# Optimization experiments

Measured on AMD Instinct MI355X. Metric: run time of the kernel, lower is better.

The kernel has to match this reference:

```python
import jax, jax.numpy as jnp
import numpy as np

N, E, D, H, C, ED = 30000, 300000, 256, 8, 32, 32
HID = H * C  # 256 = hidden_channels


def setup_inputs() -> dict:
    key = jax.random.key(0)
    ks = jax.random.split(key, 14)
    w = lambda k, shp, fan: (jax.random.normal(k, shp, jnp.float32) / np.sqrt(fan)).astype(jnp.float32)
    return {
        "x": jax.random.normal(ks[0], (N, D), jnp.float32),
        "edge_index": jax.random.randint(ks[1], (2, E), 0, N, jnp.int32),
        "edge_attr": jax.random.normal(ks[2], (E, ED), jnp.float32),
        # TransformerConv params (PyG: q/k/v Linears have bias; lin_edge & lin_skip bias=False)
        "Wq": w(ks[3], (D, HID), D), "bq": 0.01 * jax.random.normal(ks[4], (HID,), jnp.float32),
        "Wk": w(ks[5], (D, HID), D), "bk": 0.01 * jax.random.normal(ks[6], (HID,), jnp.float32),
        "Wv": w(ks[7], (D, HID), D), "bv": 0.01 * jax.random.normal(ks[8], (HID,), jnp.float32),
        "We": w(ks[9], (ED, HID), ED),
        "Wskip": w(ks[10], (D, HID), D),
        # MLP([HID, HID, HID], gelu-tanh, plain_last=False): two Linear+act layers
        "W1": w(ks[11], (HID, HID), HID), "b1": jnp.zeros((HID,), jnp.float32),
        "W2": w(ks[12], (HID, HID), HID), "b2": jnp.zeros((HID,), jnp.float32),
    }


def reference(x, edge_index, edge_attr, Wq, bq, Wk, bk, Wv, bv, We, Wskip, W1, b1, W2, b2):
    src, dst = edge_index[0], edge_index[1]  # message flows src -> dst
    q = (x @ Wq + bq).reshape(N, H, C)
    k = (x @ Wk + bk).reshape(N, H, C)
    v = (x @ Wv + bv).reshape(N, H, C)
    e = (edge_attr @ We).reshape(E, H, C)
    k_e = k[src] + e                               # [E,H,C]
    v_e = v[src] + e                               # [E,H,C]
    logits = jnp.einsum('ehc,ehc->eh', q[dst], k_e) / np.sqrt(C)  # [E,H]
    # segment softmax over incoming edges of each dst node
    m = jax.ops.segment_max(logits, dst, num_segments=N)          # [N,H]
    a = jnp.exp(logits - m[dst])
    denom = jax.ops.segment_sum(a, dst, num_segments=N)           # [N,H]
    alpha = a / (denom[dst] + 1e-16)                              # [E,H]
    agg = jax.ops.segment_sum(alpha[:, :, None] * v_e, dst, num_segments=N)  # [N,H,C]
    out = agg.reshape(N, HID) + x @ Wskip          # concat heads + root skip
    # residual MLP: x + gelu(gelu(x W1 + b1) W2 + b2)
    h = jax.nn.gelu(out @ W1 + b1, approximate=True)
    h = jax.nn.gelu(h @ W2 + b2, approximate=True)
    return out + h
```

## Files before the change

### kernel.cpp

```cpp
#include <hip/hip_runtime.h>

#define NN 30000
#define NE 300000
#define HIDDEN 256

typedef __attribute__((ext_vector_type(8))) __bf16 bf16x8;
typedef __attribute__((ext_vector_type(4))) __bf16 bf16x4;
typedef __attribute__((ext_vector_type(4))) float float4v;

__device__ inline __bf16 f2bf(float f) {
  unsigned u = __builtin_bit_cast(unsigned, f);
  u += 0x7fffu + ((u >> 16) & 1u);
  unsigned short s = (unsigned short)(u >> 16);
  return __builtin_bit_cast(__bf16, s);
}
__device__ inline float bf2f(__bf16 b) {
  unsigned short s = __builtin_bit_cast(unsigned short, b);
  unsigned u = ((unsigned)s) << 16;
  return __builtin_bit_cast(float, u);
}
__device__ inline float gelu_tanh(float x) {
  float x3 = x * x * x;
  return 0.5f * x * (1.0f + tanhf(0.79788456080286536f * (x + 0.044715f * x3)));
}

__global__ __launch_bounds__(256) void prep_kernel(
    const float* __restrict__ Wq, const float* __restrict__ Wk, const float* __restrict__ Wv,
    const float* __restrict__ Wsk, const float* __restrict__ W1, const float* __restrict__ W2,
    const float* __restrict__ We, const float* __restrict__ bq, const float* __restrict__ bk,
    const float* __restrict__ bv, const float* __restrict__ x,
    __bf16* __restrict__ WTall, __bf16* __restrict__ WT1, __bf16* __restrict__ WT2,
    float* __restrict__ ball, float* __restrict__ WeT, __bf16* __restrict__ xb) {
  const int b = blockIdx.x;
  const int tid = threadIdx.x;
  if (b < 1792) {
    const int region = b >> 8;
    const int idx = ((b & 255) << 8) | tid;
    const int k = idx & 255, n = idx >> 8;
    float v;
    if (region == 3) {
      const int h = n >> 5, d = n & 31;
      const float* wq = Wq + (size_t)k * 256 + h * 32;
      const float* we = We + (size_t)d * 256 + h * 32;
      float s = 0.f;
#pragma unroll
      for (int c = 0; c < 32; ++c) s += wq[c] * we[c];
      v = s;
    } else {
      const float* W = (region == 0) ? Wq : (region == 1) ? Wk : (region == 2) ? Wv
                     : (region == 4) ? Wsk : (region == 5) ? W1 : W2;
      v = W[(size_t)k * 256 + n];
    }
    const __bf16 bv16 = f2bf(v);
    if (region < 5) WTall[(size_t)region * 65536 + idx] = bv16;
    else if (region == 5) WT1[idx] = bv16;
    else WT2[idx] = bv16;
  } else if (b < 1797) {
    const int j = (b - 1792) * 256 + tid;
    if (j < 1280) {
      float v = 0.f;
      if (j < 256) v = bq[j];
      else if (j < 512) v = bk[j - 256];
      else if (j < 768) v = bv[j - 512];
      else if (j < 1024) {
        const int col = j - 768, h = col >> 5, d = col & 31;
        const float* bqh = bq + h * 32;
        const float* we = We + (size_t)d * 256 + h * 32;
        float s = 0.f;
#pragma unroll
        for (int c = 0; c < 32; ++c) s += bqh[c] * we[c];
        v = s;
      }
      ball[j] = v;
    }
  } else if (b < 1829) {
    const int idx = (b - 1797) * 256 + tid;
    const int ch = idx >> 5, d = idx & 31;
    WeT[idx] = We[(size_t)d * 256 + ch];
  } else {
    const int t = (b - 1829) * 256 + tid;
    if (t < NN * 256 / 8) {
      const float* p = x + (size_t)t * 8;
      float4v f0 = *(const float4v*)(p);
      float4v f1 = *(const float4v*)(p + 4);
      bf16x8 o;
#pragma unroll
      for (int j = 0; j < 4; ++j) { o[j] = f2bf(f0[j]); o[j + 4] = f2bf(f1[j]); }
      *(bf16x8*)(xb + (size_t)t * 8) = o;
    }
  }
}

__global__ void zero_int_kernel(int* __restrict__ p, int n) {
  int i = blockIdx.x * 256 + threadIdx.x;
  if (i < n) p[i] = 0;
}

__global__ void count_deg_kernel(const int* __restrict__ dst, int* __restrict__ deg, int E) {
  int e = blockIdx.x * 256 + threadIdx.x;
  if (e < E) atomicAdd(&deg[dst[e]], 1);
}

__global__ __launch_bounds__(1024) void scan_kernel(const int* __restrict__ deg,
                                                    int* __restrict__ offs, int n) {
  __shared__ int part[1024];
  const int tid = threadIdx.x;
  const int per = (n + 1023) / 1024;
  const int base = tid * per;
  int s = 0;
  for (int j = 0; j < per; ++j) {
    int i = base + j;
    if (i < n) s += deg[i];
  }
  part[tid] = s;
  __syncthreads();
  for (int st = 1; st < 1024; st <<= 1) {
    int t = (tid >= st) ? part[tid - st] : 0;
    __syncthreads();
    part[tid] += t;
    __syncthreads();
  }
  int run = (tid > 0) ? part[tid - 1] : 0;
  for (int j = 0; j < per; ++j) {
    int i = base + j;
    if (i < n) { offs[i] = run; run += deg[i]; }
  }
  if (tid == 1023) offs[n] = part[1023];
}

__global__ void scatter_kernel(const int* __restrict__ srcIn, const int* __restrict__ dstIn,
                               const int* __restrict__ offs, int* __restrict__ cursor,
                               int* __restrict__ srcs, int* __restrict__ eids, int E) {
  int e = blockIdx.x * 256 + threadIdx.x;
  if (e >= E) return;
  int d = dstIn[e];
  int p = atomicAdd(&cursor[d], 1);
  int o = offs[d] + p;
  srcs[o] = srcIn[e];
  eids[o] = e;
}

__global__ void gather_ea_kernel(const float* __restrict__ ea, const int* __restrict__ eids,
                                 __bf16* __restrict__ eaC, int E) {
  int t = blockIdx.x * 256 + threadIdx.x;
  if (t >= E * 4) return;
  int o = t >> 2, part = t & 3;
  int e = eids[o];
  const float* src = ea + (size_t)e * 32 + part * 8;
  float4v f0 = *(const float4v*)(src);
  float4v f1 = *(const float4v*)(src + 4);
  bf16x8 b;
#pragma unroll
  for (int j = 0; j < 4; ++j) { b[j] = f2bf(f0[j]); b[j + 4] = f2bf(f1[j]); }
  *(bf16x8*)(eaC + (size_t)o * 32 + part * 8) = b;
}

template <int GX, int EPI, int MODE>
__global__ __launch_bounds__(256) void gemm_k4(
    const __bf16* __restrict__ A, const __bf16* __restrict__ Wt,
    const float* __restrict__ bias,
    float* __restrict__ Yf, __bf16* __restrict__ Ybf,
    __bf16* __restrict__ QGp, __bf16* __restrict__ KVp,
    const float* __restrict__ resid, int M, int gyTiles) {
  __shared__ char smem[128 * 264 * 2];
  __bf16* Bs = (__bf16*)smem;
  const int bid = blockIdx.x;
  const int stripe = bid / (8 * GX);
  const int rem = bid % (8 * GX);
  const int y8 = rem % 8;
  const int xt = rem / 8;
  const int y = stripe * 8 + y8;
  if (y >= gyTiles) return;
  const int n0 = xt * 128;

  {
    const int t = threadIdx.x;
#pragma unroll
    for (int i = 0; i < 16; ++i) {
      int g = i * 256 + t;
      int row = g >> 5;
      int c16 = g & 31;
      bf16x8 v = *(const bf16x8*)(Wt + (size_t)(n0 + row) * 256 + c16 * 8);
      *(bf16x8*)(Bs + row * 264 + c16 * 8) = v;
    }
  }
  __syncthreads();

  const int lane = threadIdx.x & 63;
  const int w = threadIdx.x >> 6;
  const int r = lane & 15;
  const int q = lane >> 4;
  const int mw = y * 128 + w * 32;
  int ar0 = mw + r;      if (ar0 >= M) ar0 = M - 1;
  int ar1 = mw + 16 + r; if (ar1 >= M) ar1 = M - 1;
  const int kq = q * 8;

  float4v acc[2][8];
#pragma unroll
  for (int i = 0; i < 2; ++i)
#pragma unroll
    for (int t = 0; t < 8; ++t) acc[i][t] = (float4v){0.f, 0.f, 0.f, 0.f};

#pragma unroll
  for (int kk = 0; kk < 256; kk += 32) {
    const int ka = kk + kq;
    bf16x8 a0 = *(const bf16x8*)(A + (size_t)ar0 * 256 + ka);
    bf16x8 a1 = *(const bf16x8*)(A + (size_t)ar1 * 256 + ka);
    bf16x8 b[8];
#pragma unroll
    for (int t = 0; t < 8; ++t)
      b[t] = *(const bf16x8*)(Bs + (t * 16 + r) * 264 + ka);
#pragma unroll
    for (int t = 0; t < 8; ++t) {
      acc[0][t] = __builtin_amdgcn_mfma_f32_16x16x32_bf16(a0, b[t], acc[0][t], 0, 0, 0);
      acc[1][t] = __builtin_amdgcn_mfma_f32_16x16x32_bf16(a1, b[t], acc[1][t], 0, 0, 0);
    }
  }
  __syncthreads();

  float* cs = (float*)smem + w * 4224;
#pragma unroll
  for (int t = 0; t < 8; ++t) {
    const int col = n0 + t * 16 + r;
    const float bb = bias ? bias[col] : 0.0f;
#pragma unroll
    for (int i2 = 0; i2 < 2; ++i2)
#pragma unroll
      for (int ii = 0; ii < 4; ++ii) {
        float v = acc[i2][t][ii] + bb;
        if constexpr (EPI == 2 || EPI == 3) v = gelu_tanh(v);
        cs[(i2 * 16 + q * 4 + ii) * 132 + t * 16 + r] = v;
      }
  }

  constexpr int NSTR = GX * 128;
  const int p = n0 >> 8;
  const int cbase = n0 & 255;
  __bf16* dstI = (p == 0 || p == 3) ? QGp : KVp;
  const int moff = (p >= 2) ? 4 : 0;
#pragma unroll
  for (int i = 0; i < 16; ++i) {
    const int rl = i * 2 + (lane >> 5);
    const int row = mw + rl;
    const int c4 = (lane & 31) * 4;
    float4v v = *(const float4v*)(cs + rl * 132 + c4);
    if (row < M) {
      if constexpr (MODE == 1) {
        if (p == 4) {
          *(float4v*)(Yf + (size_t)row * 256 + cbase + c4) = v;
        } else {
          bf16x4 b4;
          b4[0] = f2bf(v[0]); b4[1] = f2bf(v[1]); b4[2] = f2bf(v[2]); b4[3] = f2bf(v[3]);
          const int c = cbase + c4;
          *(bf16x4*)(dstI + (size_t)row * 512 + 2 * c + moff) = b4;
        }
      } else if constexpr (EPI == 1) {
        *(float4v*)(Yf + (size_t)row * NSTR + n0 + c4) = v;
      } else if constexpr (EPI == 3) {
        float4v rr = *(const float4v*)(resid + (size_t)row * NSTR + n0 + c4);
        v[0] += rr[0]; v[1] += rr[1]; v[2] += rr[2]; v[3] += rr[3];
        *(float4v*)(Yf + (size_t)row * NSTR + n0 + c4) = v;
      } else {
        bf16x4 b4;
        b4[0] = f2bf(v[0]); b4[1] = f2bf(v[1]); b4[2] = f2bf(v[2]); b4[3] = f2bf(v[3]);
        *(bf16x4*)(Ybf + (size_t)row * NSTR + n0 + c4) = b4;
      }
    }
  }
}

__global__ __launch_bounds__(256) void attn_kernel(
    const __bf16* __restrict__ QG, const __bf16* __restrict__ KV,
    const __bf16* __restrict__ eaC,
    const int* __restrict__ offs, const int* __restrict__ srcs,
    float* __restrict__ OUT, __bf16* __restrict__ AE) {
  __shared__ float sdn[4][64];
  __shared__ float sav[4][64][4], sae[4][64][4];
  const int lane = threadIdx.x & 63;
  const int w = threadIdx.x >> 6;
  const int n = blockIdx.x;
  const int c0 = lane * 4;
  const int sub = lane & 7;

  const bf16x8 qg = *(const bf16x8*)(QG + (size_t)n * 512 + lane * 8);
  const float q0 = bf2f(qg[0]), q1 = bf2f(qg[1]), q2 = bf2f(qg[2]), q3 = bf2f(qg[3]);
  const float g0 = bf2f(qg[4]), g1 = bf2f(qg[5]), g2 = bf2f(qg[6]), g3 = bf2f(qg[7]);

  float denom = 0.f;
  float4v accv = {0.f, 0.f, 0.f, 0.f};
  float4v acce = {0.f, 0.f, 0.f, 0.f};
  const int beg = offs[n], end = offs[n + 1];
  for (int i = beg + w; i < end; i += 4) {
    const int sn = srcs[i];
    const bf16x8 kv = *(const bf16x8*)(KV + (size_t)sn * 512 + lane * 8);
    const bf16x4 e4 = *(const bf16x4*)(eaC + (size_t)i * 32 + sub * 4);
    const float e0 = bf2f(e4[0]), e1 = bf2f(e4[1]), e2 = bf2f(e4[2]), e3 = bf2f(e4[3]);
    float part = q0 * bf2f(kv[0]) + q1 * bf2f(kv[1]) + q2 * bf2f(kv[2]) + q3 * bf2f(kv[3])
               + g0 * e0 + g1 * e1 + g2 * e2 + g3 * e3;
    part += __shfl_xor(part, 1);
    part += __shfl_xor(part, 2);
    part += __shfl_xor(part, 4);
    const float wgt = __expf(part * 0.17677669529663687f);
    denom += wgt;
    accv[0] += wgt * bf2f(kv[4]);
    accv[1] += wgt * bf2f(kv[5]);
    accv[2] += wgt * bf2f(kv[6]);
    accv[3] += wgt * bf2f(kv[7]);
    acce[0] += wgt * e0;
    acce[1] += wgt * e1;
    acce[2] += wgt * e2;
    acce[3] += wgt * e3;
  }
  sdn[w][lane] = denom;
#pragma unroll
  for (int j = 0; j < 4; ++j) { sav[w][lane][j] = accv[j]; sae[w][lane][j] = acce[j]; }
  __syncthreads();
  if (w == 0) {
    float D = 0.f;
    float4v av = {0.f, 0.f, 0.f, 0.f};
    float4v ae = {0.f, 0.f, 0.f, 0.f};
#pragma unroll
    for (int ww = 0; ww < 4; ++ww) {
      D += sdn[ww][lane];
#pragma unroll
      for (int j = 0; j < 4; ++j) { av[j] += sav[ww][lane][j]; ae[j] += sae[ww][lane][j]; }
    }
    const float inv = 1.0f / (D + 1e-16f);
    float4v o = *(const float4v*)(OUT + (size_t)n * 256 + c0);
#pragma unroll
    for (int j = 0; j < 4; ++j) o[j] += av[j] * inv;
    *(float4v*)(OUT + (size_t)n * 256 + c0) = o;
    bf16x4 aeb;
    aeb[0] = f2bf(ae[0] * inv); aeb[1] = f2bf(ae[1] * inv);
    aeb[2] = f2bf(ae[2] * inv); aeb[3] = f2bf(ae[3] * inv);
    *(bf16x4*)(AE + (size_t)n * 256 + c0) = aeb;
  }
}

__global__ __launch_bounds__(256) void post_kernel(
    const __bf16* __restrict__ AE, const float* __restrict__ WeT,
    float* __restrict__ OUT, __bf16* __restrict__ OUTh) {
  const int lane = threadIdx.x & 63;
  const int wave = threadIdx.x >> 6;
  const int c0 = lane * 4;
  const int hg = lane >> 3;

  float4v w4[4][8];
#pragma unroll
  for (int j = 0; j < 4; ++j)
#pragma unroll
    for (int s = 0; s < 8; ++s)
      w4[j][s] = *(const float4v*)(WeT + (size_t)(c0 + j) * 32 + s * 4);

  const int nbase = blockIdx.x * 64;
  for (int it = 0; it < 16; ++it) {
    const int n = nbase + it * 4 + wave;
    if (n >= NN) return;
    const __bf16* aerow = AE + (size_t)n * HIDDEN + hg * 32;
    float aef[32];
#pragma unroll
    for (int t = 0; t < 4; ++t) {
      bf16x8 a8 = *(const bf16x8*)(aerow + t * 8);
#pragma unroll
      for (int j = 0; j < 8; ++j) aef[t * 8 + j] = bf2f(a8[j]);
    }
    float4v o = *(const float4v*)(OUT + (size_t)n * HIDDEN + c0);
#pragma unroll
    for (int j = 0; j < 4; ++j) {
      float s = 0.f;
#pragma unroll
      for (int g = 0; g < 8; ++g) {
        s += aef[g * 4 + 0] * w4[j][g][0] + aef[g * 4 + 1] * w4[j][g][1]
           + aef[g * 4 + 2] * w4[j][g][2] + aef[g * 4 + 3] * w4[j][g][3];
      }
      o[j] += s;
    }
    *(float4v*)(OUT + (size_t)n * HIDDEN + c0) = o;
    bf16x4 ob;
    ob[0] = f2bf(o[0]); ob[1] = f2bf(o[1]); ob[2] = f2bf(o[2]); ob[3] = f2bf(o[3]);
    *(bf16x4*)(OUTh + (size_t)n * HIDDEN + c0) = ob;
  }
}

extern "C" void kernel_launch(void* const* d_in, const int* in_sizes, int n_in,
                              void* d_out, int out_size, void* d_ws, size_t ws_size,
                              hipStream_t stream) {
  (void)in_sizes; (void)n_in; (void)out_size; (void)ws_size;
  const float* x   = (const float*)d_in[0];
  const int*   ei  = (const int*)d_in[1];
  const float* ea  = (const float*)d_in[2];
  const float* Wq  = (const float*)d_in[3];
  const float* bq  = (const float*)d_in[4];
  const float* Wk  = (const float*)d_in[5];
  const float* bk  = (const float*)d_in[6];
  const float* Wv  = (const float*)d_in[7];
  const float* bv  = (const float*)d_in[8];
  const float* We  = (const float*)d_in[9];
  const float* Wsk = (const float*)d_in[10];
  const float* W1  = (const float*)d_in[11];
  const float* b1  = (const float*)d_in[12];
  const float* W2  = (const float*)d_in[13];
  const float* b2  = (const float*)d_in[14];
  float* out = (float*)d_out;

  char* ws = (char*)d_ws;
  size_t off = 0;
  auto alloc = [&](size_t bytes) -> char* {
    off = (off + 255) & ~(size_t)255;
    char* p = ws + off;
    off += bytes;
    return p;
  };
  __bf16* QG   = (__bf16*)alloc((size_t)NN * 512 * 2);
  __bf16* KV   = (__bf16*)alloc((size_t)NN * 512 * 2);
  __bf16* xb   = (__bf16*)alloc((size_t)NN * 256 * 2);
  __bf16* AE   = (__bf16*)alloc((size_t)NN * 256 * 2);
  __bf16* OUTh = (__bf16*)alloc((size_t)NN * 256 * 2);
  __bf16* eaC  = (__bf16*)alloc((size_t)NE * 32 * 2);
  __bf16* WTall = (__bf16*)alloc((size_t)1280 * 256 * 2);
  __bf16* WT1  = (__bf16*)alloc(256 * 256 * 2);
  __bf16* WT2  = (__bf16*)alloc(256 * 256 * 2);
  float*  ball = (float*)alloc(1280 * 4);
  float*  WeT  = (float*)alloc(256 * 32 * 4);
  int* deg    = (int*)alloc((size_t)2 * NN * 4);
  int* cursor = deg + NN;
  int* offs   = (int*)alloc((size_t)(NN + 1) * 4);
  int* srcs   = (int*)alloc((size_t)NE * 4);
  int* eids   = (int*)alloc((size_t)NE * 4);
  __bf16* H1 = AE;

  const int* srcIn = ei;
  const int* dstIn = ei + NE;

  const int prepBlocks = 1829 + (NN * 256 / 8 + 255) / 256;
  prep_kernel<<<prepBlocks, 256, 0, stream>>>(Wq, Wk, Wv, Wsk, W1, W2, We, bq, bk, bv, x,
                                              WTall, WT1, WT2, ball, WeT, xb);

  zero_int_kernel<<<(2 * NN + 255) / 256, 256, 0, stream>>>(deg, 2 * NN);
  count_deg_kernel<<<(NE + 255) / 256, 256, 0, stream>>>(dstIn, deg, NE);
  scan_kernel<<<1, 1024, 0, stream>>>(deg, offs, NN);
  scatter_kernel<<<(NE + 255) / 256, 256, 0, stream>>>(srcIn, dstIn, offs, cursor, srcs, eids, NE);
  gather_ea_kernel<<<(NE * 4 + 255) / 256, 256, 0, stream>>>(ea, eids, eaC, NE);

  const int gy = (NN + 127) / 128;
  const int stripes = (gy + 7) / 8;
  gemm_k4<10, 0, 1><<<stripes * 80, 256, 0, stream>>>(
      xb, WTall, ball, out, nullptr, QG, KV, nullptr, NN, gy);

  attn_kernel<<<NN, 256, 0, stream>>>(QG, KV, eaC, offs, srcs, out, AE);

  post_kernel<<<(NN + 63) / 64, 256, 0, stream>>>(AE, WeT, out, OUTh);

  gemm_k4<2, 2, 0><<<stripes * 16, 256, 0, stream>>>(
      OUTh, WT1, b1, nullptr, H1, nullptr, nullptr, nullptr, NN, gy);
  gemm_k4<2, 3, 0><<<stripes * 16, 256, 0, stream>>>(
      H1, WT2, b2, out, nullptr, nullptr, nullptr, out, NN, gy);
}
```

Measured before the change: 404.4 us.

## Parallelize CSR scan, pack src/eid pairs, drop edge gather, one wave per node attention

Replaces the single-block serial scan with a three-kernel multi-block prefix sum, and folds degree zeroing into the prep kernel. The scatter step now writes packed (src, eid) pairs, and the separate bf16 edge-attribute gather kernel is removed. The attention kernel reads fp32 edge_attr directly by edge id. It now assigns one wave per destination node instead of four waves per node, which removes the shared-memory reduction and block barrier, and unrolls the edge loop by two using exp2. In exchange, edge-attribute reads become random and twice as wide, and high-degree nodes are processed serially by a single wave.

```diff
diff --git a/kernel.cpp b/kernel.cpp
--- a/kernel.cpp
+++ b/kernel.cpp
@@ -24,13 +24,15 @@
   return 0.5f * x * (1.0f + tanhf(0.79788456080286536f * (x + 0.044715f * x3)));
 }
 
+#define PREP_XB_END (1829 + (NN * 32 + 255) / 256)
 __global__ __launch_bounds__(256) void prep_kernel(
     const float* __restrict__ Wq, const float* __restrict__ Wk, const float* __restrict__ Wv,
     const float* __restrict__ Wsk, const float* __restrict__ W1, const float* __restrict__ W2,
     const float* __restrict__ We, const float* __restrict__ bq, const float* __restrict__ bk,
     const float* __restrict__ bv, const float* __restrict__ x,
     __bf16* __restrict__ WTall, __bf16* __restrict__ WT1, __bf16* __restrict__ WT2,
-    float* __restrict__ ball, float* __restrict__ WeT, __bf16* __restrict__ xb) {
+    float* __restrict__ ball, float* __restrict__ WeT, __bf16* __restrict__ xb,
+    int* __restrict__ degz) {
   const int b = blockIdx.x;
   const int tid = threadIdx.x;
   if (b < 1792) {
@@ -77,7 +79,7 @@
     const int idx = (b - 1797) * 256 + tid;
     const int ch = idx >> 5, d = idx & 31;
     WeT[idx] = We[(size_t)d * 256 + ch];
-  } else {
+  } else if (b < PREP_XB_END) {
     const int t = (b - 1829) * 256 + tid;
     if (t < NN * 256 / 8) {
       const float* p = x + (size_t)t * 8;
@@ -88,12 +90,10 @@
       for (int j = 0; j < 4; ++j) { o[j] = f2bf(f0[j]); o[j + 4] = f2bf(f1[j]); }
       *(bf16x8*)(xb + (size_t)t * 8) = o;
     }
-  }
-}
-
-__global__ void zero_int_kernel(int* __restrict__ p, int n) {
-  int i = blockIdx.x * 256 + threadIdx.x;
-  if (i < n) p[i] = 0;
+  } else {
+    const int idx = (b - PREP_XB_END) * 256 + tid;
+    if (idx < 2 * NN) degz[idx] = 0;
+  }
 }
 
 __global__ void count_deg_kernel(const int* __restrict__ dst, int* __restrict__ deg, int E) {
@@ -101,58 +101,61 @@
   if (e < E) atomicAdd(&deg[dst[e]], 1);
 }
 
-__global__ __launch_bounds__(1024) void scan_kernel(const int* __restrict__ deg,
-                                                    int* __restrict__ offs, int n) {
-  __shared__ int part[1024];
-  const int tid = threadIdx.x;
-  const int per = (n + 1023) / 1024;
-  const int base = tid * per;
-  int s = 0;
-  for (int j = 0; j < per; ++j) {
-    int i = base + j;
-    if (i < n) s += deg[i];
-  }
-  part[tid] = s;
+__global__ __launch_bounds__(256) void deg_psum_kernel(const int* __restrict__ deg,
+                                                       int* __restrict__ psum, int n) {
+  int i = blockIdx.x * 256 + threadIdx.x;
+  int v = (i < n) ? deg[i] : 0;
+#pragma unroll
+  for (int s = 1; s < 64; s <<= 1) v += __shfl_xor(v, s);
+  __shared__ int ws[4];
+  if ((threadIdx.x & 63) == 0) ws[threadIdx.x >> 6] = v;
   __syncthreads();
-  for (int st = 1; st < 1024; st <<= 1) {
-    int t = (tid >= st) ? part[tid - st] : 0;
+  if (threadIdx.x == 0) psum[blockIdx.x] = ws[0] + ws[1] + ws[2] + ws[3];
+}
+
+__global__ __launch_bounds__(128) void psum_scan_kernel(int* __restrict__ psum,
+                                                        int* __restrict__ offs, int nb) {
+  __shared__ int tmp[128];
+  const int t = threadIdx.x;
+  int v = (t < nb) ? psum[t] : 0;
+  tmp[t] = v;
+  __syncthreads();
+  for (int s = 1; s < 128; s <<= 1) {
+    int u = (t >= s) ? tmp[t - s] : 0;
     __syncthreads();
-    part[tid] += t;
+    tmp[t] += u;
     __syncthreads();
   }
-  int run = (tid > 0) ? part[tid - 1] : 0;
-  for (int j = 0; j < per; ++j) {
-    int i = base + j;
-    if (i < n) { offs[i] = run; run += deg[i]; }
-  }
-  if (tid == 1023) offs[n] = part[1023];
+  if (t < nb) psum[t] = tmp[t] - v;
+  if (t == 0) offs[NN] = NE;
+}
+
+__global__ __launch_bounds__(256) void offs_kernel(const int* __restrict__ deg,
+                                                   const int* __restrict__ psum,
+                                                   int* __restrict__ offs, int n) {
+  __shared__ int tmp[256];
+  const int t = threadIdx.x;
+  const int i = blockIdx.x * 256 + t;
+  int v = (i < n) ? deg[i] : 0;
+  tmp[t] = v;
+  __syncthreads();
+  for (int s = 1; s < 256; s <<= 1) {
+    int u = (t >= s) ? tmp[t - s] : 0;
+    __syncthreads();
+    tmp[t] += u;
+    __syncthreads();
+  }
+  if (i < n) offs[i] = psum[blockIdx.x] + tmp[t] - v;
 }
 
 __global__ void scatter_kernel(const int* __restrict__ srcIn, const int* __restrict__ dstIn,
                                const int* __restrict__ offs, int* __restrict__ cursor,
-                               int* __restrict__ srcs, int* __restrict__ eids, int E) {
+                               int2* __restrict__ sed, int E) {
   int e = blockIdx.x * 256 + threadIdx.x;
   if (e >= E) return;
   int d = dstIn[e];
   int p = atomicAdd(&cursor[d], 1);
-  int o = offs[d] + p;
-  srcs[o] = srcIn[e];
-  eids[o] = e;
-}
-
-__global__ void gather_ea_kernel(const float* __restrict__ ea, const int* __restrict__ eids,
-                                 __bf16* __restrict__ eaC, int E) {
-  int t = blockIdx.x * 256 + threadIdx.x;
-  if (t >= E * 4) return;
-  int o = t >> 2, part = t & 3;
-  int e = eids[o];
-  const float* src = ea + (size_t)e * 32 + part * 8;
-  float4v f0 = *(const float4v*)(src);
-  float4v f1 = *(const float4v*)(src + 4);
-  bf16x8 b;
-#pragma unroll
-  for (int j = 0; j < 4; ++j) { b[j] = f2bf(f0[j]); b[j + 4] = f2bf(f1[j]); }
-  *(bf16x8*)(eaC + (size_t)o * 32 + part * 8) = b;
+  sed[offs[d] + p] = make_int2(srcIn[e], e);
 }
 
 template <int GX, int EPI, int MODE>
@@ -271,15 +274,13 @@
 
 __global__ __launch_bounds__(256) void attn_kernel(
     const __bf16* __restrict__ QG, const __bf16* __restrict__ KV,
-    const __bf16* __restrict__ eaC,
-    const int* __restrict__ offs, const int* __restrict__ srcs,
+    const float* __restrict__ ea, const int2* __restrict__ sed,
+    const int* __restrict__ offs,
     float* __restrict__ OUT, __bf16* __restrict__ AE) {
-  __shared__ float sdn[4][64];
-  __shared__ float sav[4][64][4], sae[4][64][4];
   const int lane = threadIdx.x & 63;
   const int w = threadIdx.x >> 6;
-  const int n = blockIdx.x;
-  const int c0 = lane * 4;
+  const int n = blockIdx.x * 4 + w;
+  if (n >= NN) return;
   const int sub = lane & 7;
 
   const bf16x8 qg = *(const bf16x8*)(QG + (size_t)n * 512 + lane * 8);
@@ -290,51 +291,66 @@
   float4v accv = {0.f, 0.f, 0.f, 0.f};
   float4v acce = {0.f, 0.f, 0.f, 0.f};
   const int beg = offs[n], end = offs[n + 1];
-  for (int i = beg + w; i < end; i += 4) {
-    const int sn = srcs[i];
-    const bf16x8 kv = *(const bf16x8*)(KV + (size_t)sn * 512 + lane * 8);
-    const bf16x4 e4 = *(const bf16x4*)(eaC + (size_t)i * 32 + sub * 4);
-    const float e0 = bf2f(e4[0]), e1 = bf2f(e4[1]), e2 = bf2f(e4[2]), e3 = bf2f(e4[3]);
-    float part = q0 * bf2f(kv[0]) + q1 * bf2f(kv[1]) + q2 * bf2f(kv[2]) + q3 * bf2f(kv[3])
-               + g0 * e0 + g1 * e1 + g2 * e2 + g3 * e3;
-    part += __shfl_xor(part, 1);
-    part += __shfl_xor(part, 2);
-    part += __shfl_xor(part, 4);
-    const float wgt = __expf(part * 0.17677669529663687f);
-    denom += wgt;
-    accv[0] += wgt * bf2f(kv[4]);
-    accv[1] += wgt * bf2f(kv[5]);
-    accv[2] += wgt * bf2f(kv[6]);
-    accv[3] += wgt * bf2f(kv[7]);
-    acce[0] += wgt * e0;
-    acce[1] += wgt * e1;
-    acce[2] += wgt * e2;
-    acce[3] += wgt * e3;
-  }
-  sdn[w][lane] = denom;
-#pragma unroll
-  for (int j = 0; j < 4; ++j) { sav[w][lane][j] = accv[j]; sae[w][lane][j] = acce[j]; }
-  __syncthreads();
-  if (w == 0) {
-    float D = 0.f;
-    float4v av = {0.f, 0.f, 0.f, 0.f};
-    float4v ae = {0.f, 0.f, 0.f, 0.f};
-#pragma unroll
-    for (int ww = 0; ww < 4; ++ww) {
-      D += sdn[ww][lane];
-#pragma unroll
-      for (int j = 0; j < 4; ++j) { av[j] += sav[ww][lane][j]; ae[j] += sae[ww][lane][j]; }
-    }
-    const float inv = 1.0f / (D + 1e-16f);
-    float4v o = *(const float4v*)(OUT + (size_t)n * 256 + c0);
-#pragma unroll
-    for (int j = 0; j < 4; ++j) o[j] += av[j] * inv;
-    *(float4v*)(OUT + (size_t)n * 256 + c0) = o;
-    bf16x4 aeb;
-    aeb[0] = f2bf(ae[0] * inv); aeb[1] = f2bf(ae[1] * inv);
-    aeb[2] = f2bf(ae[2] * inv); aeb[3] = f2bf(ae[3] * inv);
-    *(bf16x4*)(AE + (size_t)n * 256 + c0) = aeb;
-  }
+  const float LSC = 0.25506589858f;
+
+  int i = beg;
+  for (; i + 2 <= end; i += 2) {
+    const int2 s0 = sed[i];
+    const int2 s1 = sed[i + 1];
+    const bf16x8 kv0 = *(const bf16x8*)(KV + (size_t)s0.x * 512 + lane * 8);
+    const float4v e0 = *(const float4v*)(ea + (size_t)s0.y * 32 + sub * 4);
+    const bf16x8 kv1 = *(const bf16x8*)(KV + (size_t)s1.x * 512 + lane * 8);
+    const float4v e1 = *(const float4v*)(ea + (size_t)s1.y * 32 + sub * 4);
+    float p0 = q0 * bf2f(kv0[0]) + q1 * bf2f(kv0[1]) + q2 * bf2f(kv0[2]) + q3 * bf2f(kv0[3])
+             + g0 * e0[0] + g1 * e0[1] + g2 * e0[2] + g3 * e0[3];
+    float p1 = q0 * bf2f(kv1[0]) + q1 * bf2f(kv1[1]) + q2 * bf2f(kv1[2]) + q3 * bf2f(kv1[3])
+             + g0 * e1[0] + g1 * e1[1] + g2 * e1[2] + g3 * e1[3];
+    p0 += __shfl_xor(p0, 1); p1 += __shfl_xor(p1, 1);
+    p0 += __shfl_xor(p0, 2); p1 += __shfl_xor(p1, 2);
+    p0 += __shfl_xor(p0, 4); p1 += __shfl_xor(p1, 4);
+    const float w0 = exp2f(p0 * LSC);
+    const float w1 = exp2f(p1 * LSC);
+    denom += w0 + w1;
+    accv[0] += w0 * bf2f(kv0[4]) + w1 * bf2f(kv1[4]);
+    accv[1] += w0 * bf2f(kv0[5]) + w1 * bf2f(kv1[5]);
+    accv[2] += w0 * bf2f(kv0[6]) + w1 * bf2f(kv1[6]);
+    accv[3] += w0 * bf2f(kv0[7]) + w1 * bf2f(kv1[7]);
+    acce[0] += w0 * e0[0] + w1 * e1[0];
+    acce[1] += w0 * e0[1] + w1 * e1[1];
+    acce[2] += w0 * e0[2] + w1 * e1[2];
+    acce[3] += w0 * e0[3] + w1 * e1[3];
+  }
+  if (i < end) {
+    const int2 s0 = sed[i];
+    const bf16x8 kv0 = *(const bf16x8*)(KV + (size_t)s0.x * 512 + lane * 8);
+    const float4v e0 = *(const float4v*)(ea + (size_t)s0.y * 32 + sub * 4);
+    float p0 = q0 * bf2f(kv0[0]) + q1 * bf2f(kv0[1]) + q2 * bf2f(kv0[2]) + q3 * bf2f(kv0[3])
+             + g0 * e0[0] + g1 * e0[1] + g2 * e0[2] + g3 * e0[3];
+    p0 += __shfl_xor(p0, 1);
+    p0 += __shfl_xor(p0, 2);
+    p0 += __shfl_xor(p0, 4);
+    const float w0 = exp2f(p0 * LSC);
+    denom += w0;
+    accv[0] += w0 * bf2f(kv0[4]);
+    accv[1] += w0 * bf2f(kv0[5]);
+    accv[2] += w0 * bf2f(kv0[6]);
+    accv[3] += w0 * bf2f(kv0[7]);
+    acce[0] += w0 * e0[0];
+    acce[1] += w0 * e0[1];
+    acce[2] += w0 * e0[2];
+    acce[3] += w0 * e0[3];
+  }
+
+  const float inv = 1.0f / (denom + 1e-16f);
+  const int c0 = lane * 4;
+  float4v o = *(const float4v*)(OUT + (size_t)n * 256 + c0);
+#pragma unroll
+  for (int j = 0; j < 4; ++j) o[j] += accv[j] * inv;
+  *(float4v*)(OUT + (size_t)n * 256 + c0) = o;
+  bf16x4 aeb;
+  aeb[0] = f2bf(acce[0] * inv); aeb[1] = f2bf(acce[1] * inv);
+  aeb[2] = f2bf(acce[2] * inv); aeb[3] = f2bf(acce[3] * inv);
+  *(bf16x4*)(AE + (size_t)n * 256 + c0) = aeb;
 }
 
 __global__ __launch_bounds__(256) void post_kernel(
@@ -416,7 +432,6 @@
   __bf16* xb   = (__bf16*)alloc((size_t)NN * 256 * 2);
   __bf16* AE   = (__bf16*)alloc((size_t)NN * 256 * 2);
   __bf16* OUTh = (__bf16*)alloc((size_t)NN * 256 * 2);
-  __bf16* eaC  = (__bf16*)alloc((size_t)NE * 32 * 2);
   __bf16* WTall = (__bf16*)alloc((size_t)1280 * 256 * 2);
   __bf16* WT1  = (__bf16*)alloc(256 * 256 * 2);
   __bf16* WT2  = (__bf16*)alloc(256 * 256 * 2);
@@ -425,29 +440,30 @@
   int* deg    = (int*)alloc((size_t)2 * NN * 4);
   int* cursor = deg + NN;
   int* offs   = (int*)alloc((size_t)(NN + 1) * 4);
-  int* srcs   = (int*)alloc((size_t)NE * 4);
-  int* eids   = (int*)alloc((size_t)NE * 4);
+  int* psum   = (int*)alloc(512);
+  int2* sed   = (int2*)alloc((size_t)NE * 8);
   __bf16* H1 = AE;
 
   const int* srcIn = ei;
   const int* dstIn = ei + NE;
 
-  const int prepBlocks = 1829 + (NN * 256 / 8 + 255) / 256;
+  const int prepBlocks = PREP_XB_END + (2 * NN + 255) / 256;
   prep_kernel<<<prepBlocks, 256, 0, stream>>>(Wq, Wk, Wv, Wsk, W1, W2, We, bq, bk, bv, x,
-                                              WTall, WT1, WT2, ball, WeT, xb);
-
-  zero_int_kernel<<<(2 * NN + 255) / 256, 256, 0, stream>>>(deg, 2 * NN);
+                                              WTall, WT1, WT2, ball, WeT, xb, deg);
+
+  const int nb = (NN + 255) / 256;
   count_deg_kernel<<<(NE + 255) / 256, 256, 0, stream>>>(dstIn, deg, NE);
-  scan_kernel<<<1, 1024, 0, stream>>>(deg, offs, NN);
-  scatter_kernel<<<(NE + 255) / 256, 256, 0, stream>>>(srcIn, dstIn, offs, cursor, srcs, eids, NE);
-  gather_ea_kernel<<<(NE * 4 + 255) / 256, 256, 0, stream>>>(ea, eids, eaC, NE);
+  deg_psum_kernel<<<nb, 256, 0, stream>>>(deg, psum, NN);
+  psum_scan_kernel<<<1, 128, 0, stream>>>(psum, offs, nb);
+  offs_kernel<<<nb, 256, 0, stream>>>(deg, psum, offs, NN);
+  scatter_kernel<<<(NE + 255) / 256, 256, 0, stream>>>(srcIn, dstIn, offs, cursor, sed, NE);
 
   const int gy = (NN + 127) / 128;
   const int stripes = (gy + 7) / 8;
   gemm_k4<10, 0, 1><<<stripes * 80, 256, 0, stream>>>(
       xb, WTall, ball, out, nullptr, QG, KV, nullptr, NN, gy);
 
-  attn_kernel<<<NN, 256, 0, stream>>>(QG, KV, eaC, offs, srcs, out, AE);
+  attn_kernel<<<(NN + 3) / 4, 256, 0, stream>>>(QG, KV, ea, sed, offs, out, AE);
 
   post_kernel<<<(NN + 63) / 64, 256, 0, stream>>>(AE, WeT, out, OUTh);
 
```

Result: faster. 364.0 us (-10.0%).
